# Kernel tuning notes

Hardware: AMD Instinct MI355X
Metric: run time of the kernel (lower is better)

The kernel has to match this reference:

```python
import jax, jax.numpy as jnp
import numpy as np

B, S, T = 32, 64, 64
D, H = 256, 512
VIN, VOUT = 32000, 32000


def _p(key, shape, scale=0.1):
    return scale * jax.random.normal(key, shape, dtype=jnp.float32)


def setup_inputs() -> dict:
    key = jax.random.key(0)
    ks = jax.random.split(key, 32)
    inp = {}
    inp["input_seq"] = jax.random.randint(ks[0], (B, S), 0, VIN, dtype=jnp.int32)
    inp["target_seq"] = jax.random.randint(ks[1], (B, T), 0, VOUT, dtype=jnp.int32)
    # encoder params
    inp["E_enc"] = _p(ks[2], (VIN, D))
    inp["Wx_e0"] = _p(ks[3], (3 * H, D)); inp["Wh_e0"] = _p(ks[4], (3 * H, H))
    inp["bx_e0"] = _p(ks[5], (3 * H,)); inp["bh_e0"] = _p(ks[6], (3 * H,))
    inp["Wx_e1"] = _p(ks[7], (3 * H, H)); inp["Wh_e1"] = _p(ks[8], (3 * H, H))
    inp["bx_e1"] = _p(ks[9], (3 * H,)); inp["bh_e1"] = _p(ks[10], (3 * H,))
    # decoder params
    inp["E_dec"] = _p(ks[11], (VOUT, D))
    inp["W_attn"] = _p(ks[12], (H, 2 * H)); inp["b_attn"] = _p(ks[13], (H,))
    inp["v_attn"] = jax.random.uniform(ks[14], (H,), dtype=jnp.float32)
    inp["Wx_d0"] = _p(ks[15], (3 * H, D + H)); inp["Wh_d0"] = _p(ks[16], (3 * H, H))
    inp["bx_d0"] = _p(ks[17], (3 * H,)); inp["bh_d0"] = _p(ks[18], (3 * H,))
    inp["Wx_d1"] = _p(ks[19], (3 * H, H)); inp["Wh_d1"] = _p(ks[20], (3 * H, H))
    inp["bx_d1"] = _p(ks[21], (3 * H,)); inp["bh_d1"] = _p(ks[22], (3 * H,))
    inp["W_out"] = _p(ks[23], (VOUT, H)); inp["b_out"] = _p(ks[24], (VOUT,))
    return inp


def gru_cell(h, x, Wx, Wh, bx, bh):
    # PyTorch GRU cell math: gates ordered (r, z, n)
    gi = x @ Wx.T + bx  # [B, 3H]
    gh = h @ Wh.T + bh
    i_r, i_z, i_n = jnp.split(gi, 3, axis=-1)
    h_r, h_z, h_n = jnp.split(gh, 3, axis=-1)
    r = jax.nn.sigmoid(i_r + h_r)
    z = jax.nn.sigmoid(i_z + h_z)
    n = jnp.tanh(i_n + r * h_n)
    return (1.0 - z) * n + z * h


def gru_layer(x_tbd, h0, Wx, Wh, bx, bh):
    # x_tbd: [T, B, Din] -> outputs [T, B, H], final h [B, H]
    def step(h, x):
        h = gru_cell(h, x, Wx, Wh, bx, bh)
        return h, h
    hT, ys = jax.lax.scan(step, h0, x_tbd)
    return ys, hT


def _forward(input_seq, target_seq, E_enc, Wx_e0, Wh_e0, bx_e0, bh_e0,
             Wx_e1, Wh_e1, bx_e1, bh_e1, E_dec, W_attn, b_attn, v_attn,
             Wx_d0, Wh_d0, bx_d0, bh_d0, Wx_d1, Wh_d1, bx_d1, bh_d1,
             W_out, b_out):
    # ---- Encoder ----
    emb = E_enc[input_seq]                      # [B, S, D]
    x = jnp.transpose(emb, (1, 0, 2))           # [S, B, D]
    h0_init = jnp.zeros((input_seq.shape[0], H), jnp.float32)
    y0, he0 = gru_layer(x, h0_init, Wx_e0, Wh_e0, bx_e0, bh_e0)
    y1, he1 = gru_layer(y0, h0_init, Wx_e1, Wh_e1, bx_e1, bh_e1)
    enc_out = jnp.transpose(y1, (1, 0, 2))      # [B, S, H]

    # ---- Decoder (teacher forcing) ----
    # step t consumes: t=0 -> token 0; t>0 -> target_seq[:, t-1]
    dec_tokens = jnp.concatenate(
        [jnp.zeros((target_seq.shape[0], 1), target_seq.dtype), target_seq[:, :-1]], axis=1)
    dec_emb = E_dec[dec_tokens]                 # [B, T, D]
    dec_emb = jnp.transpose(dec_emb, (1, 0, 2)) # [T, B, D]

    def dec_step(carry, emb_t):
        h0, h1 = carry
        # Bahdanau attention over encoder outputs using top-layer hidden h1
        hid = jnp.broadcast_to(h1[:, None, :], enc_out.shape)  # [B, S, H]
        energy = jnp.tanh(jnp.concatenate([hid, enc_out], axis=-1) @ W_attn.T + b_attn)
        scores = jnp.sum(v_attn * energy, axis=-1)              # [B, S]
        a = jax.nn.softmax(scores, axis=1)
        ctx = jnp.einsum('bs,bsh->bh', a, enc_out)              # [B, H]
        rnn_in = jnp.concatenate([emb_t, ctx], axis=1)          # [B, D+H]
        h0 = gru_cell(h0, rnn_in, Wx_d0, Wh_d0, bx_d0, bh_d0)
        h1 = gru_cell(h1, h0, Wx_d1, Wh_d1, bx_d1, bh_d1)
        logits = h1 @ W_out.T + b_out                           # [B, VOUT]
        return (h0, h1), logits

    _, logits = jax.lax.scan(dec_step, (he0, he1), dec_emb)     # [T, B, VOUT]
    return jnp.transpose(logits, (1, 0, 2))                     # [B, T, VOUT]


def reference(input_seq, target_seq, E_enc, Wx_e0, Wh_e0, bx_e0, bh_e0,
              Wx_e1, Wh_e1, bx_e1, bh_e1, E_dec, W_attn, b_attn, v_attn,
              Wx_d0, Wh_d0, bx_d0, bh_d0, Wx_d1, Wh_d1, bx_d1, bh_d1,
              W_out, b_out):
    return _forward(input_seq, target_seq, E_enc, Wx_e0, Wh_e0, bx_e0, bh_e0,
                    Wx_e1, Wh_e1, bx_e1, bh_e1, E_dec, W_attn, b_attn, v_attn,
                    Wx_d0, Wh_d0, bx_d0, bh_d0, Wx_d1, Wh_d1, bx_d1, bh_d1,
                    W_out, b_out)
```

## Files before the change

kernel.cpp:

```cpp
#include <hip/hip_runtime.h>
#include <cstdint>


__device__ __forceinline__ float sigm(float x) { return 1.f / (1.f + __expf(-x)); }
__device__ __forceinline__ float dot4(float4 a, float4 b) {
    return a.x * b.x + a.y * b.y + a.z * b.z + a.w * b.w;
}

__global__ void k_zero2(float* a, float* b) {
    int i = blockIdx.x * 256 + threadIdx.x;
    a[i] = 0.f; b[i] = 0.f;
}

__global__ void k_gather_enc(const int* __restrict__ seq, const float* __restrict__ E,
                             float* __restrict__ out) {
    int r = blockIdx.x;
    int s = r >> 5, b = r & 31;
    int tok = seq[b * 64 + s];
    float4 v = ((const float4*)(E + (size_t)tok * 256))[threadIdx.x];
    ((float4*)(out + (size_t)r * 256))[threadIdx.x] = v;
}
__global__ void k_gather_dec(const int* __restrict__ tgt, const float* __restrict__ E,
                             float* __restrict__ out) {
    int r = blockIdx.x;
    int t = r >> 5, b = r & 31;
    int tok = (t == 0) ? 0 : tgt[b * 64 + (t - 1)];
    float4 v = ((const float4*)(E + (size_t)tok * 256))[threadIdx.x];
    ((float4*)(out + (size_t)r * 256))[threadIdx.x] = v;
}

__global__ __launch_bounds__(256) void k_transpose4(
    const float* __restrict__ in, float* __restrict__ out,
    int W, int ldin, int coloff)
{
    __shared__ float t[32][33];
    int k0 = blockIdx.x * 32, c0 = blockIdx.y * 32;
    int tx = threadIdx.x & 31, ty = threadIdx.x >> 5;
    #pragma unroll
    for (int i = 0; i < 32; i += 8)
        t[ty + i][tx] = in[(size_t)(c0 + ty + i) * ldin + coloff + k0 + tx];
    __syncthreads();
    float4 v;
    v.x = t[tx][4 * ty + 0];
    v.y = t[tx][4 * ty + 1];
    v.z = t[tx][4 * ty + 2];
    v.w = t[tx][4 * ty + 3];
    ((float4*)out)[(size_t)((k0 >> 2) + ty) * W + c0 + tx] = v;
}

__global__ __launch_bounds__(256) void k_sgemm(
    const float* __restrict__ A, int lda,
    const float* __restrict__ W, int ldw, int coloff,
    const float* __restrict__ bias,
    float* __restrict__ outF, int N, int K, int out_mode)
{
    __shared__ float As[16][68];
    __shared__ float Ws[16][68];
    int tid = threadIdx.x;
    int tx = tid & 15, ty = tid >> 4;
    int m_base = blockIdx.y * 64;
    int n_base = blockIdx.x * 64;
    float acc[4][4] = {};

    for (int k0 = 0; k0 < K; k0 += 16) {
        #pragma unroll
        for (int i = 0; i < 4; i++) {
            int e = tid + 256 * i;
            int mm = e >> 4, kk = e & 15;
            As[kk][mm] = A[(size_t)(m_base + mm) * lda + k0 + kk];
            Ws[kk][mm] = W[(size_t)(n_base + mm) * ldw + coloff + k0 + kk];
        }
        __syncthreads();
        #pragma unroll
        for (int kk = 0; kk < 16; kk++) {
            float4 av = *(const float4*)&As[kk][ty * 4];
            float4 wv = *(const float4*)&Ws[kk][tx * 4];
            float a[4] = {av.x, av.y, av.z, av.w};
            float w[4] = {wv.x, wv.y, wv.z, wv.w};
            #pragma unroll
            for (int i = 0; i < 4; i++)
                #pragma unroll
                for (int j = 0; j < 4; j++)
                    acc[i][j] += a[i] * w[j];
        }
        __syncthreads();
    }

    #pragma unroll
    for (int j = 0; j < 4; j++) {
        int n = n_base + tx * 4 + j;
        float bv = bias ? bias[n] : 0.f;
        #pragma unroll
        for (int i = 0; i < 4; i++) {
            int m = m_base + ty * 4 + i;
            float v = acc[i][j] + bv;
            if (out_mode == 0) {
                outF[(size_t)m * N + n] = v;
            } else {
                int t = m >> 5, b = m & 31;
                outF[((size_t)(b * 64 + t)) * N + n] = v;
            }
        }
    }
}

__global__ __launch_bounds__(256) void k_gru_step(
    const float* __restrict__ gi,
    const float* __restrict__ WhT4,
    const float* __restrict__ bh,
    const float* __restrict__ hin, float* __restrict__ hout,
    float* __restrict__ yout, int ystride)
{
    __shared__ __align__(16) float hs[8][512];
    int tid = threadIdx.x;
    int il = tid & 31, bl = tid >> 5;
    int i = blockIdx.x * 32 + il;
    int b = blockIdx.y * 8 + bl;
    for (int e = tid; e < 4096; e += 256) {
        int bb = e >> 9, k = e & 511;
        hs[bb][k] = hin[(blockIdx.y * 8 + bb) * 512 + k];
    }
    __syncthreads();
    const float* hp = hs[bl];
    const float4* W4 = (const float4*)WhT4;
    float a0 = 0.f, a1 = 0.f, a2 = 0.f;
    #pragma unroll 4
    for (int k4 = 0; k4 < 128; k4++) {
        float4 h4 = *(const float4*)&hp[4 * k4];
        size_t base = (size_t)k4 * 1536 + i;
        float4 w0 = W4[base];
        float4 w1 = W4[base + 512];
        float4 w2 = W4[base + 1024];
        a0 += dot4(w0, h4); a1 += dot4(w1, h4); a2 += dot4(w2, h4);
    }
    const float* gir = gi + b * 1536;
    float gr  = gir[i]        + a0 + bh[i];
    float gz  = gir[i + 512]  + a1 + bh[i + 512];
    float gin = gir[i + 1024];
    float ghn = a2 + bh[i + 1024];
    float r = sigm(gr), z = sigm(gz);
    float n = tanhf(gin + r * ghn);
    float hnew = (1.f - z) * n + z * hp[i];
    hout[b * 512 + i] = hnew;
    yout[(size_t)b * ystride + i] = hnew;
}

__global__ __launch_bounds__(256) void k_gru_d0(
    const float* __restrict__ pregi,
    const float* __restrict__ WhT4,
    const float* __restrict__ WcT4,
    const float* __restrict__ bh,
    const float* __restrict__ ctx,
    const float* __restrict__ hin, float* __restrict__ hout)
{
    __shared__ __align__(16) float hs[8][512];
    __shared__ __align__(16) float cs[8][512];
    int tid = threadIdx.x;
    int il = tid & 31, bl = tid >> 5;
    int i = blockIdx.x * 32 + il;
    int b = blockIdx.y * 8 + bl;
    for (int e = tid; e < 4096; e += 256) {
        int bb = e >> 9, k = e & 511;
        int g = (blockIdx.y * 8 + bb) * 512 + k;
        hs[bb][k] = hin[g];
        cs[bb][k] = ctx[g];
    }
    __syncthreads();
    const float* hp = hs[bl];
    const float* cp = cs[bl];
    const float4* Wh4 = (const float4*)WhT4;
    const float4* Wc4 = (const float4*)WcT4;
    float a0 = 0.f, a1 = 0.f, a2 = 0.f, c0 = 0.f, c1 = 0.f, c2 = 0.f;
    #pragma unroll 2
    for (int k4 = 0; k4 < 128; k4++) {
        float4 h4 = *(const float4*)&hp[4 * k4];
        float4 c4 = *(const float4*)&cp[4 * k4];
        size_t base = (size_t)k4 * 1536 + i;
        float4 p0 = Wh4[base], p1 = Wh4[base + 512], p2 = Wh4[base + 1024];
        float4 q0 = Wc4[base], q1 = Wc4[base + 512], q2 = Wc4[base + 1024];
        a0 += dot4(p0, h4); a1 += dot4(p1, h4); a2 += dot4(p2, h4);
        c0 += dot4(q0, c4); c1 += dot4(q1, c4); c2 += dot4(q2, c4);
    }
    const float* gir = pregi + b * 1536;
    float gr  = gir[i]        + c0 + a0 + bh[i];
    float gz  = gir[i + 512]  + c1 + a1 + bh[i + 512];
    float gin = gir[i + 1024] + c2;
    float ghn = a2 + bh[i + 1024];
    float r = sigm(gr), z = sigm(gz);
    float n = tanhf(gin + r * ghn);
    hout[b * 512 + i] = (1.f - z) * n + z * hp[i];
}

__global__ __launch_bounds__(256) void k_gru_d1(
    const float* __restrict__ WxT4, const float* __restrict__ bx,
    const float* __restrict__ WhT4, const float* __restrict__ bh,
    const float* __restrict__ x,
    const float* __restrict__ hin, float* __restrict__ hout,
    float* __restrict__ H1step)
{
    __shared__ __align__(16) float xs[8][512];
    __shared__ __align__(16) float hs[8][512];
    int tid = threadIdx.x;
    int il = tid & 31, bl = tid >> 5;
    int i = blockIdx.x * 32 + il;
    int b = blockIdx.y * 8 + bl;
    for (int e = tid; e < 4096; e += 256) {
        int bb = e >> 9, k = e & 511;
        int g = (blockIdx.y * 8 + bb) * 512 + k;
        xs[bb][k] = x[g];
        hs[bb][k] = hin[g];
    }
    __syncthreads();
    const float* xp = xs[bl];
    const float* hp = hs[bl];
    const float4* Wx4 = (const float4*)WxT4;
    const float4* Wh4 = (const float4*)WhT4;
    float g0 = 0.f, g1 = 0.f, g2 = 0.f, a0 = 0.f, a1 = 0.f, a2 = 0.f;
    #pragma unroll 2
    for (int k4 = 0; k4 < 128; k4++) {
        float4 x4 = *(const float4*)&xp[4 * k4];
        float4 h4 = *(const float4*)&hp[4 * k4];
        size_t base = (size_t)k4 * 1536 + i;
        float4 p0 = Wx4[base], p1 = Wx4[base + 512], p2 = Wx4[base + 1024];
        float4 q0 = Wh4[base], q1 = Wh4[base + 512], q2 = Wh4[base + 1024];
        g0 += dot4(p0, x4); g1 += dot4(p1, x4); g2 += dot4(p2, x4);
        a0 += dot4(q0, h4); a1 += dot4(q1, h4); a2 += dot4(q2, h4);
    }
    float gr  = g0 + bx[i]        + a0 + bh[i];
    float gz  = g1 + bx[i + 512]  + a1 + bh[i + 512];
    float gin = g2 + bx[i + 1024];
    float ghn = a2 + bh[i + 1024];
    float r = sigm(gr), z = sigm(gz);
    float n = tanhf(gin + r * ghn);
    float hnew = (1.f - z) * n + z * hp[i];
    hout[b * 512 + i] = hnew;
    H1step[(size_t)b * 512 + i] = hnew;
}

__global__ __launch_bounds__(256) void k_attn_ph(
    const float* __restrict__ h1, const float* __restrict__ WaT4,
    float* __restrict__ ph)
{
    __shared__ __align__(16) float hs[8][512];
    int tid = threadIdx.x;
    int il = tid & 31, bl = tid >> 5;
    int j = blockIdx.x * 32 + il;
    int b = blockIdx.y * 8 + bl;
    for (int e = tid; e < 4096; e += 256) {
        int bb = e >> 9, k = e & 511;
        hs[bb][k] = h1[(blockIdx.y * 8 + bb) * 512 + k];
    }
    __syncthreads();
    const float* hp = hs[bl];
    const float4* W4 = (const float4*)WaT4;
    float a = 0.f;
    #pragma unroll 4
    for (int k4 = 0; k4 < 128; k4++) {
        float4 h4 = *(const float4*)&hp[4 * k4];
        float4 w = W4[(size_t)k4 * 512 + j];
        a += dot4(w, h4);
    }
    ph[b * 512 + j] = a;
}

__global__ __launch_bounds__(256) void k_attn_sc(
    const float* __restrict__ ph,
    const float* __restrict__ preenc,
    const float* __restrict__ enc,
    const float* __restrict__ vattn,
    float* __restrict__ ctx)
{
    __shared__ float phs[512], red[256], sc[64], aw[64];
    int b = blockIdx.x, tid = threadIdx.x;
    phs[tid]       = ph[b * 512 + tid];
    phs[tid + 256] = ph[b * 512 + tid + 256];
    __syncthreads();

    int s = tid >> 2, q = tid & 3;
    const float* pe = preenc + ((size_t)b * 64 + s) * 512;
    float part = 0.f;
    for (int h = q; h < 512; h += 4)
        part += vattn[h] * tanhf(pe[h] + phs[h]);
    red[tid] = part;
    __syncthreads();
    if (q == 0) sc[s] = red[tid] + red[tid + 1] + red[tid + 2] + red[tid + 3];
    __syncthreads();
    if (tid == 0) {
        float mx = -1e30f;
        for (int k = 0; k < 64; k++) mx = fmaxf(mx, sc[k]);
        float sum = 0.f;
        for (int k = 0; k < 64; k++) { float e = __expf(sc[k] - mx); aw[k] = e; sum += e; }
        float inv = 1.f / sum;
        for (int k = 0; k < 64; k++) aw[k] *= inv;
    }
    __syncthreads();

    #pragma unroll
    for (int jj = 0; jj < 2; jj++) {
        int j = tid + jj * 256;
        float c = 0.f;
        for (int s2 = 0; s2 < 64; s2++)
            c += aw[s2] * enc[((size_t)b * 64 + s2) * 512 + j];
        ctx[b * 512 + j] = c;
    }
}

extern "C" void kernel_launch(void* const* d_in, const int* in_sizes, int n_in,
                              void* d_out, int out_size, void* d_ws, size_t ws_size,
                              hipStream_t stream)
{
    const int*   seq    = (const int*)d_in[0];
    const int*   tgt    = (const int*)d_in[1];
    const float* E_enc  = (const float*)d_in[2];
    const float* Wx_e0  = (const float*)d_in[3];
    const float* Wh_e0  = (const float*)d_in[4];
    const float* bx_e0  = (const float*)d_in[5];
    const float* bh_e0  = (const float*)d_in[6];
    const float* Wx_e1  = (const float*)d_in[7];
    const float* Wh_e1  = (const float*)d_in[8];
    const float* bx_e1  = (const float*)d_in[9];
    const float* bh_e1  = (const float*)d_in[10];
    const float* E_dec  = (const float*)d_in[11];
    const float* W_attn = (const float*)d_in[12];
    const float* b_attn = (const float*)d_in[13];
    const float* v_attn = (const float*)d_in[14];
    const float* Wx_d0  = (const float*)d_in[15];
    const float* Wh_d0  = (const float*)d_in[16];
    const float* bx_d0  = (const float*)d_in[17];
    const float* bh_d0  = (const float*)d_in[18];
    const float* Wx_d1  = (const float*)d_in[19];
    const float* Wh_d1  = (const float*)d_in[20];
    const float* bx_d1  = (const float*)d_in[21];
    const float* bh_d1  = (const float*)d_in[22];
    const float* W_out  = (const float*)d_in[23];
    const float* b_out  = (const float*)d_in[24];
    float* out = (float*)d_out;

    char* ws = (char*)d_ws;
    size_t off = 0;
    auto alloc = [&](size_t bytes) -> void* {
        void* p = ws + off; off += (bytes + 255) & ~(size_t)255; return p;
    };
    float* emb_e   = (float*)alloc((size_t)2048 * 256 * 4);
    float* gi_buf  = (float*)alloc((size_t)2048 * 1536 * 4);
    float* y0      = (float*)alloc((size_t)2048 * 512 * 4);
    float* enc_out = (float*)alloc((size_t)2048 * 512 * 4);
    float* pre_enc = (float*)alloc((size_t)2048 * 512 * 4);
    float* emb_d   = (float*)alloc((size_t)2048 * 256 * 4);
    float* H1      = (float*)alloc((size_t)2048 * 512 * 4);
    float* hA0 = (float*)alloc(32 * 512 * 4);
    float* hB0 = (float*)alloc(32 * 512 * 4);
    float* hA1 = (float*)alloc(32 * 512 * 4);
    float* hB1 = (float*)alloc(32 * 512 * 4);
    float* ctx = (float*)alloc(32 * 512 * 4);
    float* ph  = (float*)alloc(32 * 512 * 4);
    float* WhT_e0 = (float*)alloc((size_t)1536 * 512 * 4);
    float* WhT_e1 = (float*)alloc((size_t)1536 * 512 * 4);
    float* WhT_d0 = (float*)alloc((size_t)1536 * 512 * 4);
    float* WcT_d0 = (float*)alloc((size_t)1536 * 512 * 4);
    float* WxT_d1 = (float*)alloc((size_t)1536 * 512 * 4);
    float* WhT_d1 = (float*)alloc((size_t)1536 * 512 * 4);
    float* WaT    = (float*)alloc((size_t)512 * 512 * 4);

    k_transpose4<<<dim3(16, 48), dim3(256), 0, stream>>>(Wh_e0, WhT_e0, 1536, 512, 0);
    k_transpose4<<<dim3(16, 48), dim3(256), 0, stream>>>(Wh_e1, WhT_e1, 1536, 512, 0);
    k_transpose4<<<dim3(16, 48), dim3(256), 0, stream>>>(Wh_d0, WhT_d0, 1536, 512, 0);
    k_transpose4<<<dim3(16, 48), dim3(256), 0, stream>>>(Wx_d0, WcT_d0, 1536, 768, 256);
    k_transpose4<<<dim3(16, 48), dim3(256), 0, stream>>>(Wx_d1, WxT_d1, 1536, 512, 0);
    k_transpose4<<<dim3(16, 48), dim3(256), 0, stream>>>(Wh_d1, WhT_d1, 1536, 512, 0);
    k_transpose4<<<dim3(16, 16), dim3(256), 0, stream>>>(W_attn, WaT, 512, 1024, 0);

    k_zero2<<<dim3(64), dim3(256), 0, stream>>>(hA0, hA1);

    k_gather_enc<<<dim3(2048), dim3(64), 0, stream>>>(seq, E_enc, emb_e);
    k_sgemm<<<dim3(24, 32), dim3(256), 0, stream>>>(
        emb_e, 256, Wx_e0, 256, 0, bx_e0, gi_buf, 1536, 256, 0);
    {
        float *cur = hA0, *nxt = hB0;
        for (int s = 0; s < 64; s++) {
            k_gru_step<<<dim3(16, 4), dim3(256), 0, stream>>>(
                gi_buf + (size_t)s * 32 * 1536, WhT_e0, bh_e0, cur, nxt,
                y0 + (size_t)s * 32 * 512, 512);
            float* t = cur; cur = nxt; nxt = t;
        }
    }
    k_sgemm<<<dim3(24, 32), dim3(256), 0, stream>>>(
        y0, 512, Wx_e1, 512, 0, bx_e1, gi_buf, 1536, 512, 0);
    {
        float *cur = hA1, *nxt = hB1;
        for (int s = 0; s < 64; s++) {
            k_gru_step<<<dim3(16, 4), dim3(256), 0, stream>>>(
                gi_buf + (size_t)s * 32 * 1536, WhT_e1, bh_e1, cur, nxt,
                enc_out + (size_t)s * 512, 64 * 512);
            float* t = cur; cur = nxt; nxt = t;
        }
    }

    k_sgemm<<<dim3(8, 32), dim3(256), 0, stream>>>(
        enc_out, 512, W_attn, 1024, 512, b_attn, pre_enc, 512, 512, 0);
    k_gather_dec<<<dim3(2048), dim3(64), 0, stream>>>(tgt, E_dec, emb_d);
    float* pre_gid = gi_buf;
    k_sgemm<<<dim3(24, 32), dim3(256), 0, stream>>>(
        emb_d, 256, Wx_d0, 768, 0, bx_d0, pre_gid, 1536, 256, 0);

    {
        float *c0 = hA0, *n0 = hB0, *c1 = hA1, *n1 = hB1;
        for (int t = 0; t < 64; t++) {
            k_attn_ph<<<dim3(16, 4), dim3(256), 0, stream>>>(c1, WaT, ph);
            k_attn_sc<<<dim3(32), dim3(256), 0, stream>>>(
                ph, pre_enc, enc_out, v_attn, ctx);
            k_gru_d0<<<dim3(16, 4), dim3(256), 0, stream>>>(
                pre_gid + (size_t)t * 32 * 1536, WhT_d0, WcT_d0, bh_d0, ctx, c0, n0);
            k_gru_d1<<<dim3(16, 4), dim3(256), 0, stream>>>(
                WxT_d1, bx_d1, WhT_d1, bh_d1, n0, c1, n1, H1 + (size_t)t * 32 * 512);
            float* tmp;
            tmp = c0; c0 = n0; n0 = tmp;
            tmp = c1; c1 = n1; n1 = tmp;
        }
    }

    k_sgemm<<<dim3(500, 32), dim3(256), 0, stream>>>(
        H1, 512, W_out, 512, 0, b_out, out, 32000, 512, 1);

    (void)in_sizes; (void)n_in; (void)out_size; (void)ws_size;
}
```

Measured before the change: 12.00 ms.

## Replace per-timestep GRU launches with persistent cooperative kernels using grid sync

Adds persistent cooperative kernels for the two encoder GRU layers and the decoder loop. Each runs all 64 timesteps in one launch and uses grid.sync() in place of the roughly 64–256 separate kernel launches. The decoder also restructures its step: the hidden-state matmuls for both layers and the attention projection run concurrently across 192 blocks, then attention, layer 0 and layer 1 follow. This targets launch overhead, at the cost of grid-wide barriers and some blocks idling in each phase. If the cooperative launch fails, the old per-step launches still run.

```diff
diff --git a/kernel.cpp b/kernel.cpp
--- a/kernel.cpp
+++ b/kernel.cpp
@@ -1,5 +1,8 @@
 #include <hip/hip_runtime.h>
+#include <hip/hip_cooperative_groups.h>
 #include <cstdint>
+
+namespace cg = cooperative_groups;
 
 
 __device__ __forceinline__ float sigm(float x) { return 1.f / (1.f + __expf(-x)); }
@@ -104,9 +107,255 @@
     }
 }
 
+__global__ __launch_bounds__(256, 1) void k_enc_coop(
+    const float* __restrict__ gi_all,
+    const float* __restrict__ WhT4,
+    const float* __restrict__ bh,
+    float* hA, float* hB,
+    float* __restrict__ yout, int ystep, int ybstride)
+{
+    cg::grid_group grid = cg::this_grid();
+    __shared__ __align__(16) float hsm[8][512];
+    int tid = threadIdx.x;
+    int bid = blockIdx.x;
+    int dimc = bid & 15, bg = bid >> 4;
+    int il = tid & 31, bl = tid >> 5;
+    int i = dimc * 32 + il;
+    int b = bg * 8 + bl;
+    const float4* W4 = (const float4*)WhT4;
+
+    for (int s = 0; s < 64; s++) {
+        const float* hc = (s & 1) ? hB : hA;
+        float*       hn = (s & 1) ? hA : hB;
+
+        for (int e = tid; e < 4096; e += 256) {
+            int bb = e >> 9, k = e & 511;
+            hsm[bb][k] = hc[(bg * 8 + bb) * 512 + k];
+        }
+        __syncthreads();
+        const float* hp = hsm[bl];
+        float a0 = 0.f, a1 = 0.f, a2 = 0.f;
+        #pragma unroll 4
+        for (int k4 = 0; k4 < 128; k4++) {
+            float4 h4 = *(const float4*)&hp[4 * k4];
+            size_t base = (size_t)k4 * 1536 + i;
+            a0 += dot4(W4[base], h4);
+            a1 += dot4(W4[base + 512], h4);
+            a2 += dot4(W4[base + 1024], h4);
+        }
+        const float* gir = gi_all + (size_t)s * 32 * 1536 + b * 1536;
+        float gr  = gir[i]        + a0 + bh[i];
+        float gz  = gir[i + 512]  + a1 + bh[i + 512];
+        float gin = gir[i + 1024];
+        float ghn = a2 + bh[i + 1024];
+        float r = sigm(gr), z = sigm(gz);
+        float n = tanhf(gin + r * ghn);
+        float hnew = (1.f - z) * n + z * hp[i];
+        hn[b * 512 + i] = hnew;
+        yout[(size_t)s * ystep + (size_t)b * ybstride + i] = hnew;
+        grid.sync();
+    }
+}
+
+__global__ __launch_bounds__(256, 1) void k_dec_coop(
+    const float* __restrict__ WaT4,
+    const float* __restrict__ WhTd0, const float* __restrict__ WcTd0,
+    const float* __restrict__ WxTd1, const float* __restrict__ WhTd1,
+    const float* __restrict__ bhd0, const float* __restrict__ bxd1,
+    const float* __restrict__ bhd1,
+    const float* __restrict__ pre_gid,
+    const float* __restrict__ pre_enc,
+    const float* __restrict__ enc,
+    const float* __restrict__ vattn,
+    float* hA0, float* hB0, float* hA1, float* hB1,
+    float* __restrict__ gh0buf, float* __restrict__ gh1buf,
+    float* __restrict__ phbuf, float* __restrict__ ctxbuf,
+    float* __restrict__ H1)
+{
+    cg::grid_group grid = cg::this_grid();
+    __shared__ __align__(16) float sm[8192];
+    int tid = threadIdx.x;
+    int bid = blockIdx.x;
+
+    for (int t = 0; t < 64; t++) {
+        const float* h0c = (t & 1) ? hB0 : hA0;
+        float*       h0n = (t & 1) ? hA0 : hB0;
+        const float* h1c = (t & 1) ? hB1 : hA1;
+        float*       h1n = (t & 1) ? hA1 : hB1;
+
+        if (bid < 128) {
+            bool is0 = bid < 64;
+            int r = is0 ? bid : bid - 64;
+            const float* W  = is0 ? WhTd0 : WhTd1;
+            const float* bh = is0 ? bhd0 : bhd1;
+            const float* hc = is0 ? h0c : h1c;
+            float* gh = is0 ? gh0buf : gh1buf;
+            int dimc = r & 15, bg = r >> 4;
+            int il = tid & 31, bl = tid >> 5;
+            int i = dimc * 32 + il;
+            int b = bg * 8 + bl;
+            float (*hs)[512] = (float(*)[512])sm;
+            for (int e = tid; e < 4096; e += 256) {
+                int bb = e >> 9, k = e & 511;
+                hs[bb][k] = hc[(bg * 8 + bb) * 512 + k];
+            }
+            __syncthreads();
+            const float* hp = hs[bl];
+            const float4* W4 = (const float4*)W;
+            float a0 = 0.f, a1 = 0.f, a2 = 0.f;
+            #pragma unroll 4
+            for (int k4 = 0; k4 < 128; k4++) {
+                float4 h4 = *(const float4*)&hp[4 * k4];
+                size_t base = (size_t)k4 * 1536 + i;
+                a0 += dot4(W4[base], h4);
+                a1 += dot4(W4[base + 512], h4);
+                a2 += dot4(W4[base + 1024], h4);
+            }
+            gh[b * 1536 + i]        = a0 + bh[i];
+            gh[b * 1536 + i + 512]  = a1 + bh[i + 512];
+            gh[b * 1536 + i + 1024] = a2 + bh[i + 1024];
+        } else {
+            int r = bid - 128;
+            int dimc = r & 15, bg = r >> 4;
+            int il = tid & 31, bl = tid >> 5;
+            int j = dimc * 32 + il;
+            float (*hs)[512] = (float(*)[512])sm;
+            for (int e = tid; e < 4096; e += 256) {
+                int bb = e >> 9, k = e & 511;
+                hs[bb][k] = h1c[(bg * 8 + bb) * 512 + k];
+            }
+            __syncthreads();
+            const float* hp = hs[bl];
+            const float4* W4 = (const float4*)WaT4;
+            float a = 0.f;
+            #pragma unroll 4
+            for (int k4 = 0; k4 < 128; k4++) {
+                float4 h4 = *(const float4*)&hp[4 * k4];
+                a += dot4(W4[(size_t)k4 * 512 + j], h4);
+            }
+            phbuf[(bg * 8 + bl) * 512 + j] = a;
+        }
+        grid.sync();
+
+        if (bid < 32) {
+            float* phs = sm;
+            float* red = sm + 512;
+            float* sc  = sm + 768;
+            float* aw  = sm + 832;
+            int b = bid;
+            phs[tid]       = phbuf[b * 512 + tid];
+            phs[tid + 256] = phbuf[b * 512 + tid + 256];
+            __syncthreads();
+            int s = tid >> 2, q = tid & 3;
+            const float* pe = pre_enc + ((size_t)b * 64 + s) * 512;
+            float part = 0.f;
+            for (int h = q; h < 512; h += 4)
+                part += vattn[h] * tanhf(pe[h] + phs[h]);
+            red[tid] = part;
+            __syncthreads();
+            if (q == 0) sc[s] = red[tid] + red[tid + 1] + red[tid + 2] + red[tid + 3];
+            __syncthreads();
+            if (tid == 0) {
+                float mx = -1e30f;
+                for (int k = 0; k < 64; k++) mx = fmaxf(mx, sc[k]);
+                float sum = 0.f;
+                for (int k = 0; k < 64; k++) { float e = __expf(sc[k] - mx); aw[k] = e; sum += e; }
+                float inv = 1.f / sum;
+                for (int k = 0; k < 64; k++) aw[k] *= inv;
+            }
+            __syncthreads();
+            #pragma unroll
+            for (int jj = 0; jj < 2; jj++) {
+                int j = tid + jj * 256;
+                float c = 0.f;
+                for (int s2 = 0; s2 < 64; s2++)
+                    c += aw[s2] * enc[((size_t)b * 64 + s2) * 512 + j];
+                ctxbuf[b * 512 + j] = c;
+            }
+        }
+        grid.sync();
+
+        if (bid < 64) {
+            int dimc = bid & 15, bg = bid >> 4;
+            int il = tid & 31, bl = tid >> 5;
+            int i = dimc * 32 + il;
+            int b = bg * 8 + bl;
+            float (*hs)[512] = (float(*)[512])sm;
+            float (*cs)[512] = (float(*)[512])(sm + 4096);
+            for (int e = tid; e < 4096; e += 256) {
+                int bb = e >> 9, k = e & 511;
+                int g = (bg * 8 + bb) * 512 + k;
+                hs[bb][k] = h0c[g];
+                cs[bb][k] = ctxbuf[g];
+            }
+            __syncthreads();
+            const float* hp = hs[bl];
+            const float* cp = cs[bl];
+            const float4* Wc4 = (const float4*)WcTd0;
+            float c0 = 0.f, c1 = 0.f, c2 = 0.f;
+            #pragma unroll 4
+            for (int k4 = 0; k4 < 128; k4++) {
+                float4 c4 = *(const float4*)&cp[4 * k4];
+                size_t base = (size_t)k4 * 1536 + i;
+                c0 += dot4(Wc4[base], c4);
+                c1 += dot4(Wc4[base + 512], c4);
+                c2 += dot4(Wc4[base + 1024], c4);
+            }
+            const float* gir = pre_gid + (size_t)t * 32 * 1536 + b * 1536;
+            const float* g0r = gh0buf + b * 1536;
+            float gr  = gir[i]        + c0 + g0r[i];
+            float gz  = gir[i + 512]  + c1 + g0r[i + 512];
+            float gin = gir[i + 1024] + c2;
+            float ghn = g0r[i + 1024];
+            float r = sigm(gr), z = sigm(gz);
+            float n = tanhf(gin + r * ghn);
+            h0n[b * 512 + i] = (1.f - z) * n + z * hp[i];
+        }
+        grid.sync();
+
+        if (bid < 64) {
+            int dimc = bid & 15, bg = bid >> 4;
+            int il = tid & 31, bl = tid >> 5;
+            int i = dimc * 32 + il;
+            int b = bg * 8 + bl;
+            float (*xs)[512] = (float(*)[512])sm;
+            float (*hs)[512] = (float(*)[512])(sm + 4096);
+            for (int e = tid; e < 4096; e += 256) {
+                int bb = e >> 9, k = e & 511;
+                int g = (bg * 8 + bb) * 512 + k;
+                xs[bb][k] = h0n[g];
+                hs[bb][k] = h1c[g];
+            }
+            __syncthreads();
+            const float* xp = xs[bl];
+            const float* hp = hs[bl];
+            const float4* Wx4 = (const float4*)WxTd1;
+            float g0 = 0.f, g1 = 0.f, g2 = 0.f;
+            #pragma unroll 4
+            for (int k4 = 0; k4 < 128; k4++) {
+                float4 x4 = *(const float4*)&xp[4 * k4];
+                size_t base = (size_t)k4 * 1536 + i;
+                g0 += dot4(Wx4[base], x4);
+                g1 += dot4(Wx4[base + 512], x4);
+                g2 += dot4(Wx4[base + 1024], x4);
+            }
+            const float* g1r = gh1buf + b * 1536;
+            float gr  = g0 + bxd1[i]        + g1r[i];
+            float gz  = g1 + bxd1[i + 512]  + g1r[i + 512];
+            float gin = g2 + bxd1[i + 1024];
+            float ghn = g1r[i + 1024];
+            float r = sigm(gr), z = sigm(gz);
+            float n = tanhf(gin + r * ghn);
+            float hnew = (1.f - z) * n + z * hp[i];
+            h1n[b * 512 + i] = hnew;
+            H1[(size_t)t * 32 * 512 + b * 512 + i] = hnew;
+        }
+        grid.sync();
+    }
+}
+
 __global__ __launch_bounds__(256) void k_gru_step(
-    const float* __restrict__ gi,
-    const float* __restrict__ WhT4,
+    const float* __restrict__ gi, const float* __restrict__ WhT4,
     const float* __restrict__ bh,
     const float* __restrict__ hin, float* __restrict__ hout,
     float* __restrict__ yout, int ystride)
@@ -128,10 +377,9 @@
     for (int k4 = 0; k4 < 128; k4++) {
         float4 h4 = *(const float4*)&hp[4 * k4];
         size_t base = (size_t)k4 * 1536 + i;
-        float4 w0 = W4[base];
-        float4 w1 = W4[base + 512];
-        float4 w2 = W4[base + 1024];
-        a0 += dot4(w0, h4); a1 += dot4(w1, h4); a2 += dot4(w2, h4);
+        a0 += dot4(W4[base], h4);
+        a1 += dot4(W4[base + 512], h4);
+        a2 += dot4(W4[base + 1024], h4);
     }
     const float* gir = gi + b * 1536;
     float gr  = gir[i]        + a0 + bh[i];
@@ -146,10 +394,8 @@
 }
 
 __global__ __launch_bounds__(256) void k_gru_d0(
-    const float* __restrict__ pregi,
-    const float* __restrict__ WhT4,
-    const float* __restrict__ WcT4,
-    const float* __restrict__ bh,
+    const float* __restrict__ pregi, const float* __restrict__ WhT4,
+    const float* __restrict__ WcT4, const float* __restrict__ bh,
     const float* __restrict__ ctx,
     const float* __restrict__ hin, float* __restrict__ hout)
 {
@@ -176,10 +422,8 @@
         float4 h4 = *(const float4*)&hp[4 * k4];
         float4 c4 = *(const float4*)&cp[4 * k4];
         size_t base = (size_t)k4 * 1536 + i;
-        float4 p0 = Wh4[base], p1 = Wh4[base + 512], p2 = Wh4[base + 1024];
-        float4 q0 = Wc4[base], q1 = Wc4[base + 512], q2 = Wc4[base + 1024];
-        a0 += dot4(p0, h4); a1 += dot4(p1, h4); a2 += dot4(p2, h4);
-        c0 += dot4(q0, c4); c1 += dot4(q1, c4); c2 += dot4(q2, c4);
+        a0 += dot4(Wh4[base], h4); a1 += dot4(Wh4[base + 512], h4); a2 += dot4(Wh4[base + 1024], h4);
+        c0 += dot4(Wc4[base], c4); c1 += dot4(Wc4[base + 512], c4); c2 += dot4(Wc4[base + 1024], c4);
     }
     const float* gir = pregi + b * 1536;
     float gr  = gir[i]        + c0 + a0 + bh[i];
@@ -221,10 +465,8 @@
         float4 x4 = *(const float4*)&xp[4 * k4];
         float4 h4 = *(const float4*)&hp[4 * k4];
         size_t base = (size_t)k4 * 1536 + i;
-        float4 p0 = Wx4[base], p1 = Wx4[base + 512], p2 = Wx4[base + 1024];
-        float4 q0 = Wh4[base], q1 = Wh4[base + 512], q2 = Wh4[base + 1024];
-        g0 += dot4(p0, x4); g1 += dot4(p1, x4); g2 += dot4(p2, x4);
-        a0 += dot4(q0, h4); a1 += dot4(q1, h4); a2 += dot4(q2, h4);
+        g0 += dot4(Wx4[base], x4); g1 += dot4(Wx4[base + 512], x4); g2 += dot4(Wx4[base + 1024], x4);
+        a0 += dot4(Wh4[base], h4); a1 += dot4(Wh4[base + 512], h4); a2 += dot4(Wh4[base + 1024], h4);
     }
     float gr  = g0 + bx[i]        + a0 + bh[i];
     float gz  = g1 + bx[i + 512]  + a1 + bh[i + 512];
@@ -257,17 +499,14 @@
     #pragma unroll 4
     for (int k4 = 0; k4 < 128; k4++) {
         float4 h4 = *(const float4*)&hp[4 * k4];
-        float4 w = W4[(size_t)k4 * 512 + j];
-        a += dot4(w, h4);
+        a += dot4(W4[(size_t)k4 * 512 + j], h4);
     }
     ph[b * 512 + j] = a;
 }
 
 __global__ __launch_bounds__(256) void k_attn_sc(
-    const float* __restrict__ ph,
-    const float* __restrict__ preenc,
-    const float* __restrict__ enc,
-    const float* __restrict__ vattn,
+    const float* __restrict__ ph, const float* __restrict__ preenc,
+    const float* __restrict__ enc, const float* __restrict__ vattn,
     float* __restrict__ ctx)
 {
     __shared__ float phs[512], red[256], sc[64], aw[64];
@@ -275,7 +514,6 @@
     phs[tid]       = ph[b * 512 + tid];
     phs[tid + 256] = ph[b * 512 + tid + 256];
     __syncthreads();
-
     int s = tid >> 2, q = tid & 3;
     const float* pe = preenc + ((size_t)b * 64 + s) * 512;
     float part = 0.f;
@@ -294,7 +532,6 @@
         for (int k = 0; k < 64; k++) aw[k] *= inv;
     }
     __syncthreads();
-
     #pragma unroll
     for (int jj = 0; jj < 2; jj++) {
         int j = tid + jj * 256;
@@ -354,6 +591,8 @@
     float* hB1 = (float*)alloc(32 * 512 * 4);
     float* ctx = (float*)alloc(32 * 512 * 4);
     float* ph  = (float*)alloc(32 * 512 * 4);
+    float* gh0 = (float*)alloc(32 * 1536 * 4);
+    float* gh1 = (float*)alloc(32 * 1536 * 4);
     float* WhT_e0 = (float*)alloc((size_t)1536 * 512 * 4);
     float* WhT_e1 = (float*)alloc((size_t)1536 * 512 * 4);
     float* WhT_d0 = (float*)alloc((size_t)1536 * 512 * 4);
@@ -372,10 +611,21 @@
 
     k_zero2<<<dim3(64), dim3(256), 0, stream>>>(hA0, hA1);
 
+    bool coop = true;
+
     k_gather_enc<<<dim3(2048), dim3(64), 0, stream>>>(seq, E_enc, emb_e);
     k_sgemm<<<dim3(24, 32), dim3(256), 0, stream>>>(
         emb_e, 256, Wx_e0, 256, 0, bx_e0, gi_buf, 1536, 256, 0);
     {
+        const float* a_gi = gi_buf; const float* a_w = WhT_e0; const float* a_bh = bh_e0;
+        float* a_hA = hA0; float* a_hB = hB0; float* a_y = y0;
+        int a_ystep = 32 * 512; int a_ybs = 512;
+        void* ka[] = {&a_gi, &a_w, &a_bh, &a_hA, &a_hB, &a_y, &a_ystep, &a_ybs};
+        hipError_t e = hipLaunchCooperativeKernel((const void*)k_enc_coop,
+                                                  dim3(64), dim3(256), ka, 0, stream);
+        if (e != hipSuccess) coop = false;
+    }
+    if (!coop) {
         float *cur = hA0, *nxt = hB0;
         for (int s = 0; s < 64; s++) {
             k_gru_step<<<dim3(16, 4), dim3(256), 0, stream>>>(
@@ -386,7 +636,16 @@
     }
     k_sgemm<<<dim3(24, 32), dim3(256), 0, stream>>>(
         y0, 512, Wx_e1, 512, 0, bx_e1, gi_buf, 1536, 512, 0);
-    {
+    if (coop) {
+        const float* a_gi = gi_buf; const float* a_w = WhT_e1; const float* a_bh = bh_e1;
+        float* a_hA = hA1; float* a_hB = hB1; float* a_y = enc_out;
+        int a_ystep = 512; int a_ybs = 64 * 512;
+        void* ka[] = {&a_gi, &a_w, &a_bh, &a_hA, &a_hB, &a_y, &a_ystep, &a_ybs};
+        hipError_t e = hipLaunchCooperativeKernel((const void*)k_enc_coop,
+                                                  dim3(64), dim3(256), ka, 0, stream);
+        if (e != hipSuccess) coop = false;
+    }
+    if (!coop) {
         float *cur = hA1, *nxt = hB1;
         for (int s = 0; s < 64; s++) {
             k_gru_step<<<dim3(16, 4), dim3(256), 0, stream>>>(
@@ -403,7 +662,26 @@
     k_sgemm<<<dim3(24, 32), dim3(256), 0, stream>>>(
         emb_d, 256, Wx_d0, 768, 0, bx_d0, pre_gid, 1536, 256, 0);
 
-    {
+    bool dec_done = false;
+    if (coop) {
+        const float* a_wa = WaT; const float* a_wh0 = WhT_d0; const float* a_wc0 = WcT_d0;
+        const float* a_wx1 = WxT_d1; const float* a_wh1 = WhT_d1;
+        const float* a_bh0 = bh_d0; const float* a_bx1 = bx_d1; const float* a_bh1 = bh_d1;
+        const float* a_pg = pre_gid; const float* a_pe = pre_enc; const float* a_en = enc_out;
+        const float* a_va = v_attn;
+        float* a_hA0 = hA0; float* a_hB0 = hB0; float* a_hA1 = hA1; float* a_hB1 = hB1;
+        float* a_gh0 = gh0; float* a_gh1 = gh1; float* a_ph = ph; float* a_ctx = ctx;
+        float* a_H1 = H1;
+        void* ka[] = {&a_wa, &a_wh0, &a_wc0, &a_wx1, &a_wh1,
+                      &a_bh0, &a_bx1, &a_bh1,
+                      &a_pg, &a_pe, &a_en, &a_va,
+                      &a_hA0, &a_hB0, &a_hA1, &a_hB1,
+                      &a_gh0, &a_gh1, &a_ph, &a_ctx, &a_H1};
+        hipError_t e = hipLaunchCooperativeKernel((const void*)k_dec_coop,
+                                                  dim3(192), dim3(256), ka, 0, stream);
+        if (e == hipSuccess) dec_done = true;
+    }
+    if (!dec_done) {
         float *c0 = hA0, *n0 = hB0, *c1 = hA1, *n1 = hB1;
         for (int t = 0; t < 64; t++) {
             k_attn_ph<<<dim3(16, 4), dim3(256), 0, stream>>>(c1, WaT, ph);
```

After: 21.94 ms. 82.9% more time.
